# Optimization experiments

Measured on AMD Instinct MI355X. Metric: run time of the kernel, lower is better.

Reference implementation:

```python
import jax, jax.numpy as jnp
import numpy as np

N, F, H, E = 100000, 64, 8, 1200000
D = F // H
HID = 32  # hardcoded MLP hidden width in the module


def setup_inputs() -> dict:
    key = jax.random.key(0)
    ks = jax.random.split(key, 16)
    s = 0.05
    return {
        "h": jax.random.normal(ks[0], (N, F), jnp.float32),
        "W_src": jax.random.normal(ks[1], (F, F), jnp.float32) * s,
        "b_src": jnp.zeros((F,), jnp.float32),
        "W_dst": jax.random.normal(ks[2], (F, F), jnp.float32) * s,
        "b_dst": jnp.zeros((F,), jnp.float32),
        "Wa1_src": jax.random.normal(ks[3], (F, HID), jnp.float32) * s,
        "ba1_src": jnp.zeros((HID,), jnp.float32),
        "Wa2_src": jax.random.normal(ks[4], (HID, H), jnp.float32) * s,
        "ba2_src": jnp.zeros((H,), jnp.float32),
        "Wa1_dst": jax.random.normal(ks[5], (F, HID), jnp.float32) * s,
        "ba1_dst": jnp.zeros((HID,), jnp.float32),
        "Wa2_dst": jax.random.normal(ks[6], (HID, H), jnp.float32) * s,
        "ba2_dst": jnp.zeros((H,), jnp.float32),
        "edge_index": jax.random.randint(ks[7], (2, E), 0, N, jnp.int64),
    }


def _attn_mlp(x, W1, b1, W2, b2):
    # Sequential(LeakyReLU(0.2), Linear(F,32), LeakyReLU(0.2), Linear(32,H))
    y = jax.nn.leaky_relu(x, 0.2)
    y = y @ W1 + b1
    y = jax.nn.leaky_relu(y, 0.2)
    return y @ W2 + b2


def reference(h, W_src, b_src, W_dst, b_dst,
              Wa1_src, ba1_src, Wa2_src, ba2_src,
              Wa1_dst, ba1_dst, Wa2_dst, ba2_dst,
              edge_index):
    src, dst = edge_index[0], edge_index[1]
    g_src = h @ W_src + b_src          # [N,F]
    g_dst = h @ W_dst + b_dst          # [N,F]
    msg_src = g_src[src]               # [E,F] gather
    msg = msg_src + g_dst[dst]         # [E,F]
    a_src = jax.nn.sigmoid(_attn_mlp(msg, Wa1_src, ba1_src, Wa2_src, ba2_src))[:, :, None]    # [E,H,1]
    a_dst = jax.nn.sigmoid(_attn_mlp(g_dst, Wa1_dst, ba1_dst, Wa2_dst, ba2_dst))[:, :, None]  # [N,H,1]
    agg = jax.ops.segment_sum(a_src * msg_src.reshape(E, H, D), dst, num_segments=N)          # [N,H,D]
    h_next = a_dst * g_dst.reshape(N, H, D) + agg
    return h_next.reshape(N, F)
```

## Files before the change

kernel.cpp:

```cpp
#include <hip/hip_runtime.h>
#include <hip/hip_bf16.h>
#include <hip/hip_fp16.h>

#define NF   64
#define NH   8
#define ND   8
#define NHID 32
#define XS   68
#define OS   10

typedef __attribute__((ext_vector_type(8))) short bf16x8v;
typedef __attribute__((ext_vector_type(4))) float f32x4v;

__device__ __forceinline__ float bf2f(unsigned short u) {
    union { unsigned int i; float f; } v; v.i = ((unsigned int)u) << 16; return v.f;
}
__device__ __forceinline__ unsigned short f2bf(float f) {
    __hip_bfloat16 b = __float2bfloat16(f);
    union { __hip_bfloat16 b; unsigned short u; } v; v.b = b; return v.u;
}
__device__ __forceinline__ void unpack8(uint4 u, float* o) {
    o[0] = __uint_as_float(u.x << 16); o[1] = __uint_as_float(u.x & 0xffff0000u);
    o[2] = __uint_as_float(u.y << 16); o[3] = __uint_as_float(u.y & 0xffff0000u);
    o[4] = __uint_as_float(u.z << 16); o[5] = __uint_as_float(u.z & 0xffff0000u);
    o[6] = __uint_as_float(u.w << 16); o[7] = __uint_as_float(u.w & 0xffff0000u);
}
__device__ __forceinline__ uint4 pack8(const float* f) {
    uint4 u;
    u.x = (unsigned)f2bf(f[0]) | ((unsigned)f2bf(f[1]) << 16);
    u.y = (unsigned)f2bf(f[2]) | ((unsigned)f2bf(f[3]) << 16);
    u.z = (unsigned)f2bf(f[4]) | ((unsigned)f2bf(f[5]) << 16);
    u.w = (unsigned)f2bf(f[6]) | ((unsigned)f2bf(f[7]) << 16);
    return u;
}
__device__ __forceinline__ float leaky(float x) { return fmaxf(x, 0.2f * x); }
__device__ __forceinline__ float sigmoidf(float x) { return 1.f / (1.f + __expf(-x)); }

__global__ void detect_kernel(const int* __restrict__ edge, int* __restrict__ flags) {
    if (threadIdx.x == 0 && blockIdx.x == 0) {
        int oddnz = 0;
        for (int i = 0; i < 32; i++) oddnz |= edge[2 * i + 1];
        flags[0] = (oddnz == 0) ? 1 : 0;
    }
}

__device__ __forceinline__ void load_edge(const int* __restrict__ edge, int e, int E,
                                          int wide, int& s, int& d) {
    if (wide) { s = edge[2 * e]; d = edge[2 * (E + e)]; }
    else      { s = edge[e];     d = edge[E + e]; }
}

#define WBF_TOTAL 12544
__global__ __launch_bounds__(256) void prep_weights_kernel(
    const float* __restrict__ Ws, const float* __restrict__ Wd,
    const float* __restrict__ W1d, const float* __restrict__ W1s,
    const float* __restrict__ W2s, unsigned short* __restrict__ o)
{
    int i = blockIdx.x * 256 + threadIdx.x;
    float v;
    if (i < 4096)        { int j = i;         v = Ws [(j & 63) * 64 + (j >> 6)]; }
    else if (i < 8192)   { int j = i - 4096;  v = Wd [(j & 63) * 64 + (j >> 6)]; }
    else if (i < 10240)  { int j = i - 8192;  v = W1d[(j & 63) * 32 + (j >> 6)]; }
    else if (i < 12288)  { int j = i - 10240; v = W1s[(j & 63) * 32 + (j >> 6)]; }
    else if (i < 12544)  { int j = i - 12288; v = W2s[(j & 31) * 8  + (j >> 5)]; }
    else return;
    o[i] = f2bf(v);
}

__global__ __launch_bounds__(64) void node_mfma_kernel(
    const float* __restrict__ h,
    const unsigned short* __restrict__ WsT, const float* __restrict__ b_src,
    const unsigned short* __restrict__ WdT, const float* __restrict__ b_dst,
    const unsigned short* __restrict__ W1T, const float* __restrict__ ba1,
    const float* __restrict__ Wa2, const float* __restrict__ ba2,
    unsigned short* __restrict__ g_src_out, unsigned short* __restrict__ g_dst_out,
    float* __restrict__ out, int* __restrict__ counts, int N)
{
    __shared__ __align__(16) unsigned short sX[64 * XS];
    __shared__ __align__(16) unsigned short sY[64 * XS];
    __shared__ float sW2[NHID * NH];
    __shared__ float sb2[NH];

    int lane = threadIdx.x;
    int nsub = lane & 15, quad = lane >> 4;
    int base = blockIdx.x * 64;
    int n = base + lane;
    bool valid = n < N;
    size_t nn = valid ? (size_t)n : (size_t)(N - 1);

    if (valid && counts) counts[n] = 0;
    for (int i = lane; i < NHID * NH; i += 64) sW2[i] = Wa2[i];
    if (lane < NH) sb2[lane] = ba2[lane];

    {
        const float4* hv = (const float4*)(h + nn * NF);
        unsigned short* xrow = sX + lane * XS;
        #pragma unroll
        for (int k = 0; k < 8; k++) {
            float4 u0 = hv[2 * k], u1 = hv[2 * k + 1];
            float f[8] = { u0.x, u0.y, u0.z, u0.w, u1.x, u1.y, u1.z, u1.w };
            uint4 p = pack8(f);
            uint2* q = (uint2*)(xrow + k * 8);
            q[0] = make_uint2(p.x, p.y);
            q[1] = make_uint2(p.z, p.w);
        }
    }
    __syncthreads();

    #pragma unroll 1
    for (int m = 0; m < 2; m++) {
        const unsigned short* WT = m ? WdT : WsT;
        const float* bb = m ? b_dst : b_src;
        unsigned short* gout = m ? g_dst_out : g_src_out;

        bf16x8v Bf[2][4];
        #pragma unroll
        for (int ks = 0; ks < 2; ks++)
            #pragma unroll
            for (int nt = 0; nt < 4; nt++) {
                union { uint4 u; bf16x8v v; } u;
                u.u = *(const uint4*)(WT + (nt * 16 + nsub) * 64 + ks * 32 + quad * 8);
                Bf[ks][nt] = u.v;
            }

        f32x4v acc[4][4];
        #pragma unroll
        for (int mt = 0; mt < 4; mt++)
            #pragma unroll
            for (int nt = 0; nt < 4; nt++) {
                f32x4v z = {0.f, 0.f, 0.f, 0.f};
                acc[mt][nt] = z;
            }

        #pragma unroll
        for (int ks = 0; ks < 2; ks++)
            #pragma unroll
            for (int mt = 0; mt < 4; mt++) {
                const unsigned short* ap = sX + (mt * 16 + nsub) * XS + ks * 32 + quad * 8;
                union { uint2 d[2]; bf16x8v v; } ua;
                ua.d[0] = *(const uint2*)ap;
                ua.d[1] = *(const uint2*)(ap + 4);
                #pragma unroll
                for (int nt = 0; nt < 4; nt++)
                    acc[mt][nt] = __builtin_amdgcn_mfma_f32_16x16x32_bf16(
                        ua.v, Bf[ks][nt], acc[mt][nt], 0, 0, 0);
            }

        if (m == 1) __syncthreads();

        #pragma unroll
        for (int nt = 0; nt < 4; nt++) {
            float bv = bb[nt * 16 + nsub];
            #pragma unroll
            for (int mt = 0; mt < 4; mt++)
                #pragma unroll
                for (int r = 0; r < 4; r++)
                    sY[(mt * 16 + quad * 4 + r) * XS + nt * 16 + nsub] =
                        f2bf(acc[mt][nt][r] + bv);
        }
        __syncthreads();

        if (valid) {
            const unsigned short* yrow = sY + lane * XS;
            uint4* gp = (uint4*)(gout + (size_t)n * NF);
            #pragma unroll
            for (int k = 0; k < 8; k++) {
                uint2 a = *(const uint2*)(yrow + k * 8);
                uint2 b = *(const uint2*)(yrow + k * 8 + 4);
                gp[k] = make_uint4(a.x, a.y, b.x, b.y);
            }
        }
    }

    bf16x8v B1f[2][2];
    #pragma unroll
    for (int ks = 0; ks < 2; ks++)
        #pragma unroll
        for (int nt = 0; nt < 2; nt++) {
            union { uint4 u; bf16x8v v; } u;
            u.u = *(const uint4*)(W1T + (nt * 16 + nsub) * 64 + ks * 32 + quad * 8);
            B1f[ks][nt] = u.v;
        }

    f32x4v acc2[4][2];
    #pragma unroll
    for (int mt = 0; mt < 4; mt++)
        #pragma unroll
        for (int nt = 0; nt < 2; nt++) {
            f32x4v z = {0.f, 0.f, 0.f, 0.f};
            acc2[mt][nt] = z;
        }

    #pragma unroll
    for (int ks = 0; ks < 2; ks++)
        #pragma unroll
        for (int mt = 0; mt < 4; mt++) {
            const unsigned short* ap = sY + (mt * 16 + nsub) * XS + ks * 32 + quad * 8;
            uint2 d0 = *(const uint2*)ap;
            uint2 d1 = *(const uint2*)(ap + 4);
            float f[8];
            unpack8(make_uint4(d0.x, d0.y, d1.x, d1.y), f);
            #pragma unroll
            for (int t = 0; t < 8; t++) f[t] = leaky(f[t]);
            uint4 p = pack8(f);
            union { uint4 u; bf16x8v v; } ua; ua.u = p;
            #pragma unroll
            for (int nt = 0; nt < 2; nt++)
                acc2[mt][nt] = __builtin_amdgcn_mfma_f32_16x16x32_bf16(
                    ua.v, B1f[ks][nt], acc2[mt][nt], 0, 0, 0);
        }
    __syncthreads();

    #pragma unroll
    for (int nt = 0; nt < 2; nt++) {
        float b1v = ba1[nt * 16 + nsub];
        #pragma unroll
        for (int mt = 0; mt < 4; mt++)
            #pragma unroll
            for (int r = 0; r < 4; r++)
                sX[(mt * 16 + quad * 4 + r) * XS + nt * 16 + nsub] =
                    f2bf(leaky(acc2[mt][nt][r] + b1v));
    }
    __syncthreads();

    if (valid) {
        float hid[NHID];
        const unsigned short* hrow = sX + lane * XS;
        #pragma unroll
        for (int k = 0; k < 8; k++) {
            uint2 dv = *(const uint2*)(hrow + k * 4);
            hid[k * 4 + 0] = bf2f((unsigned short)(dv.x & 0xffffu));
            hid[k * 4 + 1] = bf2f((unsigned short)(dv.x >> 16));
            hid[k * 4 + 2] = bf2f((unsigned short)(dv.y & 0xffffu));
            hid[k * 4 + 3] = bf2f((unsigned short)(dv.y >> 16));
        }
        float a[NH];
        #pragma unroll
        for (int j = 0; j < NH; j++) a[j] = sb2[j];
        #pragma unroll
        for (int k = 0; k < NHID; k++) {
            float xk = hid[k];
            #pragma unroll
            for (int j = 0; j < NH; j++) a[j] = fmaf(xk, sW2[k * NH + j], a[j]);
        }
        #pragma unroll
        for (int j = 0; j < NH; j++) a[j] = sigmoidf(a[j]);

        const unsigned short* yrow = sY + lane * XS;
        float4* op = (float4*)(out + (size_t)n * NF);
        #pragma unroll
        for (int k = 0; k < 8; k++) {
            uint2 u0 = *(const uint2*)(yrow + k * 8);
            uint2 u1 = *(const uint2*)(yrow + k * 8 + 4);
            float g[8];
            unpack8(make_uint4(u0.x, u0.y, u1.x, u1.y), g);
            float ah0 = a[(k * 8) >> 3];
            op[2 * k]     = make_float4(ah0 * g[0], ah0 * g[1], ah0 * g[2], ah0 * g[3]);
            op[2 * k + 1] = make_float4(ah0 * g[4], ah0 * g[5], ah0 * g[6], ah0 * g[7]);
        }
    }
}

template <bool STORE_G>
__global__ __launch_bounds__(256) void node_kernel_t(
    const float* __restrict__ h,
    const float* __restrict__ W_src, const float* __restrict__ b_src,
    const float* __restrict__ W_dst, const float* __restrict__ b_dst,
    const float* __restrict__ Wa1, const float* __restrict__ ba1,
    const float* __restrict__ Wa2, const float* __restrict__ ba2,
    unsigned short* __restrict__ g_src_out, unsigned short* __restrict__ g_dst_out,
    float* __restrict__ out, int N)
{
    __shared__ __align__(16) float sWs[NF * NF];
    __shared__ __align__(16) float sWd[NF * NF];
    __shared__ __align__(16) float sW1[NF * NHID];
    __shared__ __align__(16) float sW2[NHID * NH];
    __shared__ float sbs[NF], sbd[NF], sb1[NHID], sb2[NH];

    int tid = threadIdx.x;
    for (int i = tid; i < NF * NF; i += 256) { sWs[i] = W_src[i]; sWd[i] = W_dst[i]; }
    for (int i = tid; i < NF * NHID; i += 256) sW1[i] = Wa1[i];
    if (tid < NHID * NH) sW2[tid] = Wa2[tid];
    if (tid < NF) { sbs[tid] = b_src[tid]; sbd[tid] = b_dst[tid]; }
    if (tid < NHID) sb1[tid] = ba1[tid];
    if (tid < NH) sb2[tid] = ba2[tid];
    __syncthreads();

    int n = blockIdx.x * 256 + tid;
    if (n >= N) return;

    float hrow[NF];
    const float4* hv = (const float4*)(h + (size_t)n * NF);
    #pragma unroll
    for (int k = 0; k < 16; k++) {
        float4 u = hv[k];
        hrow[k * 4 + 0] = u.x; hrow[k * 4 + 1] = u.y;
        hrow[k * 4 + 2] = u.z; hrow[k * 4 + 3] = u.w;
    }

    float acc[NF];
    const float4* Wsv = (const float4*)sWs;
    const float4* Wdv = (const float4*)sWd;

    if (STORE_G) {
        #pragma unroll
        for (int j = 0; j < NF; j++) acc[j] = sbs[j];
        for (int i = 0; i < NF; i++) {
            float hi = hrow[i];
            #pragma unroll
            for (int jb = 0; jb < 16; jb++) {
                float4 w = Wsv[i * 16 + jb];
                acc[jb * 4 + 0] = fmaf(hi, w.x, acc[jb * 4 + 0]);
                acc[jb * 4 + 1] = fmaf(hi, w.y, acc[jb * 4 + 1]);
                acc[jb * 4 + 2] = fmaf(hi, w.z, acc[jb * 4 + 2]);
                acc[jb * 4 + 3] = fmaf(hi, w.w, acc[jb * 4 + 3]);
            }
        }
        uint4* gs = (uint4*)(g_src_out + (size_t)n * NF);
        #pragma unroll
        for (int k = 0; k < 8; k++) gs[k] = pack8(acc + k * 8);
    }

    #pragma unroll
    for (int j = 0; j < NF; j++) acc[j] = sbd[j];
    for (int i = 0; i < NF; i++) {
        float hi = hrow[i];
        #pragma unroll
        for (int jb = 0; jb < 16; jb++) {
            float4 w = Wdv[i * 16 + jb];
            acc[jb * 4 + 0] = fmaf(hi, w.x, acc[jb * 4 + 0]);
            acc[jb * 4 + 1] = fmaf(hi, w.y, acc[jb * 4 + 1]);
            acc[jb * 4 + 2] = fmaf(hi, w.z, acc[jb * 4 + 2]);
            acc[jb * 4 + 3] = fmaf(hi, w.w, acc[jb * 4 + 3]);
        }
    }
    if (STORE_G) {
        uint4* gd = (uint4*)(g_dst_out + (size_t)n * NF);
        #pragma unroll
        for (int k = 0; k < 8; k++) gd[k] = pack8(acc + k * 8);
    }

    float hid[NHID];
    #pragma unroll
    for (int j = 0; j < NHID; j++) hid[j] = sb1[j];
    const float4* W1v = (const float4*)sW1;
    for (int i = 0; i < NF; i++) {
        float xi = leaky(acc[i]);
        #pragma unroll
        for (int jb = 0; jb < 8; jb++) {
            float4 w = W1v[i * 8 + jb];
            hid[jb * 4 + 0] = fmaf(xi, w.x, hid[jb * 4 + 0]);
            hid[jb * 4 + 1] = fmaf(xi, w.y, hid[jb * 4 + 1]);
            hid[jb * 4 + 2] = fmaf(xi, w.z, hid[jb * 4 + 2]);
            hid[jb * 4 + 3] = fmaf(xi, w.w, hid[jb * 4 + 3]);
        }
    }
    float a[NH];
    #pragma unroll
    for (int j = 0; j < NH; j++) a[j] = sb2[j];
    #pragma unroll
    for (int k = 0; k < NHID; k++) {
        float xk = leaky(hid[k]);
        #pragma unroll
        for (int j = 0; j < NH; j++) a[j] = fmaf(xk, sW2[k * NH + j], a[j]);
    }
    #pragma unroll
    for (int j = 0; j < NH; j++) a[j] = sigmoidf(a[j]);

    float4* ap = (float4*)(out + (size_t)n * NF);
    #pragma unroll
    for (int k = 0; k < 16; k++) {
        int j = k * 4;
        ap[k] = make_float4(a[(j + 0) >> 3] * acc[j + 0],
                            a[(j + 1) >> 3] * acc[j + 1],
                            a[(j + 2) >> 3] * acc[j + 2],
                            a[(j + 3) >> 3] * acc[j + 3]);
    }
}

__global__ __launch_bounds__(256) void hist_kernel(
    const int* __restrict__ edge, const int* __restrict__ flags,
    int* __restrict__ counts, int* __restrict__ rank, int E, int N)
{
    int e = blockIdx.x * 256 + threadIdx.x;
    if (e >= E) return;
    int s, d;
    load_edge(edge, e, E, flags[0], s, d);
    if ((unsigned)s >= (unsigned)N || (unsigned)d >= (unsigned)N) { rank[e] = -1; return; }
    rank[e] = atomicAdd(&counts[d], 1);
}

__global__ __launch_bounds__(256) void scan1_kernel(
    const int* __restrict__ counts, int* __restrict__ offsets,
    int* __restrict__ bsums, int N)
{
    __shared__ int lds[256];
    int tid = threadIdx.x;
    int base = blockIdx.x * 2048 + tid * 8;
    int v[8]; int s = 0;
    #pragma unroll
    for (int k = 0; k < 8; k++) { int idx = base + k; int t = (idx < N) ? counts[idx] : 0; v[k] = t; s += t; }
    lds[tid] = s;
    __syncthreads();
    for (int off = 1; off < 256; off <<= 1) {
        int y = (tid >= off) ? lds[tid - off] : 0;
        __syncthreads();
        lds[tid] += y;
        __syncthreads();
    }
    int run = lds[tid] - s;
    #pragma unroll
    for (int k = 0; k < 8; k++) { int idx = base + k; if (idx < N) offsets[idx] = run; run += v[k]; }
    if (tid == 255) bsums[blockIdx.x] = lds[255];
}

__global__ void scan2_kernel(int* __restrict__ bsums, int* __restrict__ offsets, int NB, int N) {
    if (threadIdx.x == 0 && blockIdx.x == 0) {
        int run = 0;
        for (int i = 0; i < NB; i++) { int t = bsums[i]; bsums[i] = run; run += t; }
        offsets[N] = run;
    }
}

__global__ __launch_bounds__(256) void scan3_kernel(
    int* __restrict__ offsets, const int* __restrict__ bsums, int N)
{
    int add = bsums[blockIdx.x];
    int base = blockIdx.x * 2048 + threadIdx.x * 8;
    #pragma unroll
    for (int k = 0; k < 8; k++) { int idx = base + k; if (idx < N) offsets[idx] += add; }
}

__global__ __launch_bounds__(256) void scatter_kernel(
    const int* __restrict__ edge, const int* __restrict__ flags,
    const int* __restrict__ offsets, const int* __restrict__ rank,
    uint2* __restrict__ sorted_sd, int E, int N)
{
    int e = blockIdx.x * 256 + threadIdx.x;
    if (e >= E) return;
    int r = rank[e];
    if (r < 0) return;
    int s, d;
    load_edge(edge, e, E, flags[0], s, d);
    int pos = offsets[d] + r;
    sorted_sd[pos] = make_uint2((unsigned)s, (unsigned)d);
}

__global__ __launch_bounds__(256) void edge_mlp_mfma_kernel(
    const uint2* __restrict__ sorted_sd, const int* __restrict__ total_p,
    const unsigned short* __restrict__ g_src, const unsigned short* __restrict__ g_dst,
    const unsigned short* __restrict__ W1T, const float* __restrict__ ba1,
    const unsigned short* __restrict__ W2T, const float* __restrict__ ba2,
    __half* __restrict__ a_sorted)
{
    __shared__ __align__(16) unsigned short sX[4 * 64 * XS];
    __shared__ __align__(16) __half sOut[4 * 64 * OS];
    __shared__ float sb1[NHID], sb2[NH];

    int tid = threadIdx.x;
    if (tid < NHID) sb1[tid] = ba1[tid];
    if (tid < NH) sb2[tid] = ba2[tid];

    int wave = tid >> 6;
    int lane = tid & 63;
    int nsub = lane & 15;
    int quad = lane >> 4;
    int total = *total_p;
    int i = blockIdx.x * 256 + wave * 64 + lane;
    bool valid = i < total;
    uint2 sd = valid ? sorted_sd[i] : make_uint2(0u, 0u);

    unsigned short* xrow = sX + (wave * 64 + lane) * XS;
    {
        const uint4* gs = (const uint4*)(g_src + (size_t)sd.x * NF);
        const uint4* gd = (const uint4*)(g_dst + (size_t)sd.y * NF);
        #pragma unroll
        for (int k = 0; k < 8; k++) {
            float A8[8], B8[8], x8[8];
            unpack8(gs[k], A8); unpack8(gd[k], B8);
            #pragma unroll
            for (int t = 0; t < 8; t++) x8[t] = leaky(A8[t] + B8[t]);
            uint4 pk = pack8(x8);
            uint2* q = (uint2*)(xrow + k * 8);
            q[0] = make_uint2(pk.x, pk.y);
            q[1] = make_uint2(pk.z, pk.w);
        }
    }

    bf16x8v Bf[2][2];
    #pragma unroll
    for (int ks = 0; ks < 2; ks++)
        #pragma unroll
        for (int nt = 0; nt < 2; nt++) {
            union { uint4 u; bf16x8v v; } u;
            u.u = *(const uint4*)(W1T + (nt * 16 + nsub) * 64 + ks * 32 + quad * 8);
            Bf[ks][nt] = u.v;
        }
    bf16x8v B2f;
    {
        union { uint4 u; bf16x8v v; } u;
        if (nsub < NH) u.u = *(const uint4*)(W2T + nsub * 32 + quad * 8);
        else           u.u = make_uint4(0u, 0u, 0u, 0u);
        B2f = u.v;
    }

    __syncthreads();

    f32x4v acc[4][2];
    #pragma unroll
    for (int mt = 0; mt < 4; mt++)
        #pragma unroll
        for (int nt = 0; nt < 2; nt++) {
            f32x4v z = {0.f, 0.f, 0.f, 0.f};
            acc[mt][nt] = z;
        }

    const unsigned short* wbase = sX + wave * 64 * XS;
    #pragma unroll
    for (int ks = 0; ks < 2; ks++) {
        #pragma unroll
        for (int mt = 0; mt < 4; mt++) {
            const unsigned short* ap = wbase + (mt * 16 + nsub) * XS + ks * 32 + quad * 8;
            union { uint2 d[2]; bf16x8v v; } ua;
            ua.d[0] = *(const uint2*)ap;
            ua.d[1] = *(const uint2*)(ap + 4);
            #pragma unroll
            for (int nt = 0; nt < 2; nt++)
                acc[mt][nt] = __builtin_amdgcn_mfma_f32_16x16x32_bf16(
                    ua.v, Bf[ks][nt], acc[mt][nt], 0, 0, 0);
        }
    }

    __syncthreads();

    #pragma unroll
    for (int nt = 0; nt < 2; nt++) {
        int n = nt * 16 + nsub;
        float b1v = sb1[n];
        #pragma unroll
        for (int mt = 0; mt < 4; mt++) {
            #pragma unroll
            for (int r = 0; r < 4; r++) {
                int m = mt * 16 + quad * 4 + r;
                sX[(wave * 64 + m) * XS + n] = f2bf(leaky(acc[mt][nt][r] + b1v));
            }
        }
    }

    __syncthreads();

    f32x4v acc2[4];
    #pragma unroll
    for (int mt = 0; mt < 4; mt++) { f32x4v z = {0.f, 0.f, 0.f, 0.f}; acc2[mt] = z; }
    #pragma unroll
    for (int mt = 0; mt < 4; mt++) {
        const unsigned short* ap = wbase + (mt * 16 + nsub) * XS + quad * 8;
        union { uint2 d[2]; bf16x8v v; } ua;
        ua.d[0] = *(const uint2*)ap;
        ua.d[1] = *(const uint2*)(ap + 4);
        acc2[mt] = __builtin_amdgcn_mfma_f32_16x16x32_bf16(ua.v, B2f, acc2[mt], 0, 0, 0);
    }

    if (nsub < NH) {
        float b2v = sb2[nsub];
        #pragma unroll
        for (int mt = 0; mt < 4; mt++)
            #pragma unroll
            for (int r = 0; r < 4; r++) {
                int m = mt * 16 + quad * 4 + r;
                sOut[(wave * 64 + m) * OS + nsub] = __float2half(sigmoidf(acc2[mt][r] + b2v));
            }
    }
    __syncthreads();

    if (valid) {
        const unsigned int* orow = (const unsigned int*)(sOut + (wave * 64 + lane) * OS);
        uint4 pk = make_uint4(orow[0], orow[1], orow[2], orow[3]);
        *(uint4*)(a_sorted + (size_t)i * NH) = pk;
    }
}

__global__ __launch_bounds__(256) void aggregate_kernel(
    const int* __restrict__ offsets, const uint2* __restrict__ sorted_sd,
    const __half* __restrict__ a_sorted, const unsigned short* __restrict__ g_src,
    float* __restrict__ out, int N)
{
    int d = blockIdx.x * 32 + (threadIdx.x >> 3);
    if (d >= N) return;
    int l = threadIdx.x & 7;
    int beg = offsets[d], end = offsets[d + 1];

    float acc[8] = {0.f, 0.f, 0.f, 0.f, 0.f, 0.f, 0.f, 0.f};
    int i = beg;
    for (; i + 2 <= end; i += 2) {
        unsigned s0 = sorted_sd[i].x;
        unsigned s1 = sorted_sd[i + 1].x;
        float av0 = __half2float(a_sorted[(size_t)i * NH + l]);
        float av1 = __half2float(a_sorted[(size_t)(i + 1) * NH + l]);
        uint4 q0 = *(const uint4*)(g_src + (size_t)s0 * NF + l * 8);
        uint4 q1 = *(const uint4*)(g_src + (size_t)s1 * NF + l * 8);
        float f0[8], f1[8];
        unpack8(q0, f0); unpack8(q1, f1);
        #pragma unroll
        for (int t = 0; t < 8; t++) acc[t] = fmaf(av0, f0[t], acc[t]);
        #pragma unroll
        for (int t = 0; t < 8; t++) acc[t] = fmaf(av1, f1[t], acc[t]);
    }
    if (i < end) {
        unsigned s0 = sorted_sd[i].x;
        float av0 = __half2float(a_sorted[(size_t)i * NH + l]);
        uint4 q0 = *(const uint4*)(g_src + (size_t)s0 * NF + l * 8);
        float f0[8]; unpack8(q0, f0);
        #pragma unroll
        for (int t = 0; t < 8; t++) acc[t] = fmaf(av0, f0[t], acc[t]);
    }

    float4* o4 = (float4*)(out + (size_t)d * NF + l * 8);
    float4 v0 = o4[0], v1 = o4[1];
    v0.x += acc[0]; v0.y += acc[1]; v0.z += acc[2]; v0.w += acc[3];
    v1.x += acc[4]; v1.y += acc[5]; v1.z += acc[6]; v1.w += acc[7];
    o4[0] = v0; o4[1] = v1;
}

__global__ __launch_bounds__(256) void edge_kernel(
    const int* __restrict__ edge, const int* __restrict__ flags,
    const unsigned short* __restrict__ g_src, const unsigned short* __restrict__ g_dst,
    const float* __restrict__ Wa1, const float* __restrict__ ba1,
    const float* __restrict__ Wa2, const float* __restrict__ ba2,
    float* __restrict__ out, int E, int N)
{
    __shared__ __align__(16) float sW1[NF * NHID];
    __shared__ __align__(16) float sW2[NHID * NH];
    __shared__ float sb1[NHID], sb2[NH];
    int tid = threadIdx.x;
    for (int i = tid; i < NF * NHID; i += 256) sW1[i] = Wa1[i];
    if (tid < NHID * NH) sW2[tid] = Wa2[tid];
    if (tid < NHID) sb1[tid] = ba1[tid];
    if (tid < NH) sb2[tid] = ba2[tid];
    __syncthreads();

    int e = blockIdx.x * 256 + tid;
    if (e >= E) return;
    int s, d;
    load_edge(edge, e, E, flags[0], s, d);
    if ((unsigned)s >= (unsigned)N || (unsigned)d >= (unsigned)N) return;

    float ms[NF];
    float hid[NHID];
    #pragma unroll
    for (int j = 0; j < NHID; j++) hid[j] = sb1[j];

    const uint4* gs = (const uint4*)(g_src + (size_t)s * NF);
    const uint4* gd = (const uint4*)(g_dst + (size_t)d * NF);
    #pragma unroll
    for (int k = 0; k < 8; k++) {
        float a8[8], b8[8];
        unpack8(gs[k], a8);
        unpack8(gd[k], b8);
        #pragma unroll
        for (int t = 0; t < 8; t++) {
            int i = k * 8 + t;
            ms[i] = a8[t];
            float x = leaky(a8[t] + b8[t]);
            #pragma unroll
            for (int j = 0; j < NHID; j++) hid[j] = fmaf(x, sW1[i * NHID + j], hid[j]);
        }
    }

    float a[NH];
    #pragma unroll
    for (int j = 0; j < NH; j++) a[j] = sb2[j];
    #pragma unroll
    for (int k = 0; k < NHID; k++) {
        float xk = leaky(hid[k]);
        #pragma unroll
        for (int j = 0; j < NH; j++) a[j] = fmaf(xk, sW2[k * NH + j], a[j]);
    }

    float* arow = out + (size_t)d * NF;
    #pragma unroll
    for (int hh = 0; hh < NH; hh++) {
        float ah = sigmoidf(a[hh]);
        #pragma unroll
        for (int dd = 0; dd < ND; dd++)
            unsafeAtomicAdd(arow + hh * ND + dd, ah * ms[hh * ND + dd]);
    }
}

__global__ __launch_bounds__(256) void edge_kernel_fused(
    const int* __restrict__ edge, const int* __restrict__ flags,
    const float* __restrict__ h,
    const float* __restrict__ W_src, const float* __restrict__ b_src,
    const float* __restrict__ W_dst, const float* __restrict__ b_dst,
    const float* __restrict__ Wa1, const float* __restrict__ ba1,
    const float* __restrict__ Wa2, const float* __restrict__ ba2,
    float* __restrict__ out, int E, int N)
{
    __shared__ __align__(16) float sWs[NF * NF];
    __shared__ __align__(16) float sWd[NF * NF];
    __shared__ __align__(16) float sW1[NF * NHID];
    __shared__ __align__(16) float sW2[NHID * NH];
    __shared__ float sbs[NF], sbd[NF], sb1[NHID], sb2[NH];
    int tid = threadIdx.x;
    for (int i = tid; i < NF * NF; i += 256) { sWs[i] = W_src[i]; sWd[i] = W_dst[i]; }
    for (int i = tid; i < NF * NHID; i += 256) sW1[i] = Wa1[i];
    if (tid < NHID * NH) sW2[tid] = Wa2[tid];
    if (tid < NF) { sbs[tid] = b_src[tid]; sbd[tid] = b_dst[tid]; }
    if (tid < NHID) sb1[tid] = ba1[tid];
    if (tid < NH) sb2[tid] = ba2[tid];
    __syncthreads();

    int e = blockIdx.x * 256 + tid;
    if (e >= E) return;
    int wide = flags ? flags[0] : 0;
    int s, d;
    load_edge(edge, e, E, wide, s, d);
    if ((unsigned)s >= (unsigned)N || (unsigned)d >= (unsigned)N) return;

    float gsr[NF], msg[NF];
    {
        float hrow[NF];
        #pragma unroll
        for (int i = 0; i < NF; i++) hrow[i] = h[(size_t)s * NF + i];
        #pragma unroll
        for (int j = 0; j < NF; j++) gsr[j] = sbs[j];
        for (int i = 0; i < NF; i++) {
            float hi = hrow[i];
            #pragma unroll
            for (int j = 0; j < NF; j++) gsr[j] = fmaf(hi, sWs[i * NF + j], gsr[j]);
        }
    }
    #pragma unroll
    for (int j = 0; j < NF; j++) msg[j] = gsr[j] + sbd[j];
    for (int i = 0; i < NF; i++) {
        float hi = h[(size_t)d * NF + i];
        #pragma unroll
        for (int j = 0; j < NF; j++) msg[j] = fmaf(hi, sWd[i * NF + j], msg[j]);
    }

    float hid[NHID];
    #pragma unroll
    for (int j = 0; j < NHID; j++) hid[j] = sb1[j];
    for (int i = 0; i < NF; i++) {
        float x = leaky(msg[i]);
        #pragma unroll
        for (int j = 0; j < NHID; j++) hid[j] = fmaf(x, sW1[i * NHID + j], hid[j]);
    }
    float a[NH];
    #pragma unroll
    for (int j = 0; j < NH; j++) a[j] = sb2[j];
    #pragma unroll
    for (int k = 0; k < NHID; k++) {
        float xk = leaky(hid[k]);
        #pragma unroll
        for (int j = 0; j < NH; j++) a[j] = fmaf(xk, sW2[k * NH + j], a[j]);
    }

    float* arow = out + (size_t)d * NF;
    #pragma unroll
    for (int hh = 0; hh < NH; hh++) {
        float ah = sigmoidf(a[hh]);
        #pragma unroll
        for (int dd = 0; dd < ND; dd++)
            unsafeAtomicAdd(arow + hh * ND + dd, ah * gsr[hh * ND + dd]);
    }
}

static inline size_t al256(size_t x) { return (x + 255) & ~(size_t)255; }

extern "C" void kernel_launch(void* const* d_in, const int* in_sizes, int n_in,
                              void* d_out, int out_size, void* d_ws, size_t ws_size,
                              hipStream_t stream) {
    const float* h       = (const float*)d_in[0];
    const float* W_src   = (const float*)d_in[1];
    const float* b_src   = (const float*)d_in[2];
    const float* W_dst   = (const float*)d_in[3];
    const float* b_dst   = (const float*)d_in[4];
    const float* Wa1_src = (const float*)d_in[5];
    const float* ba1_src = (const float*)d_in[6];
    const float* Wa2_src = (const float*)d_in[7];
    const float* ba2_src = (const float*)d_in[8];
    const float* Wa1_dst = (const float*)d_in[9];
    const float* ba1_dst = (const float*)d_in[10];
    const float* Wa2_dst = (const float*)d_in[11];
    const float* ba2_dst = (const float*)d_in[12];
    const int* edge = (const int*)d_in[13];

    int N = in_sizes[0] / NF;
    int E = in_sizes[13] / 2;
    float* out = (float*)d_out;

    int nodeBlocks = (N + 255) / 256;
    int nodeWaves  = (N + 63) / 64;
    int edgeBlocks = (E + 255) / 256;
    int NB1 = (N + 2047) / 2048;

    size_t o_flags  = 0;
    size_t o_wbf    = al256(o_flags + 256);
    size_t o_gsrc   = al256(o_wbf + (size_t)WBF_TOTAL * 2);
    size_t o_gdst   = al256(o_gsrc + (size_t)N * NF * 2);
    size_t o_asort  = al256(o_gdst + (size_t)N * NF * 2);
    size_t o_counts = al256(o_asort + (size_t)E * NH * 2);
    size_t o_offs   = al256(o_counts + (size_t)N * 4);
    size_t o_bsums  = al256(o_offs + ((size_t)N + 1) * 4);
    size_t o_sorted = al256(o_bsums + (size_t)NB1 * 4);
    size_t need     = o_sorted + (size_t)E * 8;

    size_t gB = (size_t)N * NF * 2;

    if (ws_size >= need) {
        char* w = (char*)d_ws;
        int*            flags   = (int*)(w + o_flags);
        unsigned short* wbf     = (unsigned short*)(w + o_wbf);
        unsigned short* WsT     = wbf;
        unsigned short* WdT     = wbf + 4096;
        unsigned short* W1dT    = wbf + 8192;
        unsigned short* W1sT    = wbf + 10240;
        unsigned short* W2sT    = wbf + 12288;
        unsigned short* g_src   = (unsigned short*)(w + o_gsrc);
        unsigned short* g_dst   = (unsigned short*)(w + o_gdst);
        __half*         a_sort  = (__half*)(w + o_asort);
        int*            rank    = (int*)(w + o_asort);
        int*            counts  = (int*)(w + o_counts);
        int*            offsets = (int*)(w + o_offs);
        int*            bsums   = (int*)(w + o_bsums);
        uint2*          sorted  = (uint2*)(w + o_sorted);

        detect_kernel<<<1, 1, 0, stream>>>(edge, flags);
        prep_weights_kernel<<<(WBF_TOTAL + 255) / 256, 256, 0, stream>>>(
            W_src, W_dst, Wa1_dst, Wa1_src, Wa2_src, wbf);

        node_mfma_kernel<<<nodeWaves, 64, 0, stream>>>(
            h, WsT, b_src, WdT, b_dst,
            W1dT, ba1_dst, Wa2_dst, ba2_dst,
            g_src, g_dst, out, counts, N);

        hist_kernel<<<edgeBlocks, 256, 0, stream>>>(edge, flags, counts, rank, E, N);

        scan1_kernel<<<NB1, 256, 0, stream>>>(counts, offsets, bsums, N);
        scan2_kernel<<<1, 1, 0, stream>>>(bsums, offsets, NB1, N);
        scan3_kernel<<<NB1, 256, 0, stream>>>(offsets, bsums, N);

        scatter_kernel<<<edgeBlocks, 256, 0, stream>>>(
            edge, flags, offsets, rank, sorted, E, N);

        edge_mlp_mfma_kernel<<<edgeBlocks, 256, 0, stream>>>(
            sorted, offsets + N, g_src, g_dst,
            W1sT, ba1_src, W2sT, ba2_src, a_sort);

        aggregate_kernel<<<(N + 31) / 32, 256, 0, stream>>>(
            offsets, sorted, a_sort, g_src, out, N);
    } else if (ws_size >= 256 + 2 * gB) {
        int* flags = (int*)d_ws;
        unsigned short* g_src = (unsigned short*)((char*)d_ws + 256);
        unsigned short* g_dst = g_src + (size_t)N * NF;

        detect_kernel<<<1, 1, 0, stream>>>(edge, flags);

        node_kernel_t<true><<<nodeBlocks, 256, 0, stream>>>(
            h, W_src, b_src, W_dst, b_dst,
            Wa1_dst, ba1_dst, Wa2_dst, ba2_dst,
            g_src, g_dst, out, N);

        edge_kernel<<<edgeBlocks, 256, 0, stream>>>(
            edge, flags, g_src, g_dst,
            Wa1_src, ba1_src, Wa2_src, ba2_src,
            out, E, N);
    } else {
        int* flags = (ws_size >= 256) ? (int*)d_ws : nullptr;
        if (flags) detect_kernel<<<1, 1, 0, stream>>>(edge, flags);

        node_kernel_t<false><<<nodeBlocks, 256, 0, stream>>>(
            h, W_src, b_src, W_dst, b_dst,
            Wa1_dst, ba1_dst, Wa2_dst, ba2_dst,
            nullptr, nullptr, out, N);

        edge_kernel_fused<<<edgeBlocks, 256, 0, stream>>>(
            edge, flags, h,
            W_src, b_src, W_dst, b_dst,
            Wa1_src, ba1_src, Wa2_src, ba2_src,
            out, E, N);
    }
}
```

Before: 288.5 us.

## Fuse edge histogram into node kernel and split sorted edge arrays

Moves the per-destination edge histogram into the tail of the node MFMA kernel, and moves zeroing of counts into the weight-prep kernel. This removes one kernel launch and lets the atomics overlap with node work. The sorted (src,dst) pair array becomes separate src and dst int arrays: scatter writes only src, a new fill kernel writes dst per segment, and aggregate reads only 4 bytes per edge. In exchange there is an extra launch, the fill kernel is serialized per node, and the fused histogram loop runs on small 64-thread blocks.

```diff
diff --git a/kernel.cpp b/kernel.cpp
--- a/kernel.cpp
+++ b/kernel.cpp
@@ -54,9 +54,11 @@
 __global__ __launch_bounds__(256) void prep_weights_kernel(
     const float* __restrict__ Ws, const float* __restrict__ Wd,
     const float* __restrict__ W1d, const float* __restrict__ W1s,
-    const float* __restrict__ W2s, unsigned short* __restrict__ o)
+    const float* __restrict__ W2s, unsigned short* __restrict__ o,
+    int* __restrict__ counts, int N)
 {
     int i = blockIdx.x * 256 + threadIdx.x;
+    if (i < N) counts[i] = 0;
     float v;
     if (i < 4096)        { int j = i;         v = Ws [(j & 63) * 64 + (j >> 6)]; }
     else if (i < 8192)   { int j = i - 4096;  v = Wd [(j & 63) * 64 + (j >> 6)]; }
@@ -74,7 +76,9 @@
     const unsigned short* __restrict__ W1T, const float* __restrict__ ba1,
     const float* __restrict__ Wa2, const float* __restrict__ ba2,
     unsigned short* __restrict__ g_src_out, unsigned short* __restrict__ g_dst_out,
-    float* __restrict__ out, int* __restrict__ counts, int N)
+    float* __restrict__ out,
+    const int* __restrict__ edge, const int* __restrict__ flags,
+    int* __restrict__ counts, int* __restrict__ rank, int E, int N)
 {
     __shared__ __align__(16) unsigned short sX[64 * XS];
     __shared__ __align__(16) unsigned short sY[64 * XS];
@@ -88,7 +92,6 @@
     bool valid = n < N;
     size_t nn = valid ? (size_t)n : (size_t)(N - 1);
 
-    if (valid && counts) counts[n] = 0;
     for (int i = lane; i < NHID * NH; i += 64) sW2[i] = Wa2[i];
     if (lane < NH) sb2[lane] = ba2[lane];
 
@@ -259,6 +262,17 @@
             op[2 * k + 1] = make_float4(ah0 * g[4], ah0 * g[5], ah0 * g[6], ah0 * g[7]);
         }
     }
+
+    {
+        int wide = flags[0];
+        int stride = gridDim.x * 64;
+        for (int e = blockIdx.x * 64 + lane; e < E; e += stride) {
+            int s, d;
+            load_edge(edge, e, E, wide, s, d);
+            if ((unsigned)s >= (unsigned)N || (unsigned)d >= (unsigned)N) { rank[e] = -1; continue; }
+            rank[e] = atomicAdd(&counts[d], 1);
+        }
+    }
 }
 
 template <bool STORE_G>
@@ -378,18 +392,6 @@
     }
 }
 
-__global__ __launch_bounds__(256) void hist_kernel(
-    const int* __restrict__ edge, const int* __restrict__ flags,
-    int* __restrict__ counts, int* __restrict__ rank, int E, int N)
-{
-    int e = blockIdx.x * 256 + threadIdx.x;
-    if (e >= E) return;
-    int s, d;
-    load_edge(edge, e, E, flags[0], s, d);
-    if ((unsigned)s >= (unsigned)N || (unsigned)d >= (unsigned)N) { rank[e] = -1; return; }
-    rank[e] = atomicAdd(&counts[d], 1);
-}
-
 __global__ __launch_bounds__(256) void scan1_kernel(
     const int* __restrict__ counts, int* __restrict__ offsets,
     int* __restrict__ bsums, int N)
@@ -434,7 +436,7 @@
 __global__ __launch_bounds__(256) void scatter_kernel(
     const int* __restrict__ edge, const int* __restrict__ flags,
     const int* __restrict__ offsets, const int* __restrict__ rank,
-    uint2* __restrict__ sorted_sd, int E, int N)
+    int* __restrict__ sorted_s, int E, int N)
 {
     int e = blockIdx.x * 256 + threadIdx.x;
     if (e >= E) return;
@@ -442,12 +444,21 @@
     if (r < 0) return;
     int s, d;
     load_edge(edge, e, E, flags[0], s, d);
-    int pos = offsets[d] + r;
-    sorted_sd[pos] = make_uint2((unsigned)s, (unsigned)d);
+    sorted_s[offsets[d] + r] = s;
+}
+
+__global__ __launch_bounds__(256) void fill_d_kernel(
+    const int* __restrict__ offsets, int* __restrict__ sorted_d, int N)
+{
+    int d = blockIdx.x * 256 + threadIdx.x;
+    if (d >= N) return;
+    int beg = offsets[d], end = offsets[d + 1];
+    for (int i = beg; i < end; i++) sorted_d[i] = d;
 }
 
 __global__ __launch_bounds__(256) void edge_mlp_mfma_kernel(
-    const uint2* __restrict__ sorted_sd, const int* __restrict__ total_p,
+    const int* __restrict__ sorted_s, const int* __restrict__ sorted_d,
+    const int* __restrict__ total_p,
     const unsigned short* __restrict__ g_src, const unsigned short* __restrict__ g_dst,
     const unsigned short* __restrict__ W1T, const float* __restrict__ ba1,
     const unsigned short* __restrict__ W2T, const float* __restrict__ ba2,
@@ -468,12 +479,13 @@
     int total = *total_p;
     int i = blockIdx.x * 256 + wave * 64 + lane;
     bool valid = i < total;
-    uint2 sd = valid ? sorted_sd[i] : make_uint2(0u, 0u);
+    int s = valid ? sorted_s[i] : 0;
+    int d = valid ? sorted_d[i] : 0;
 
     unsigned short* xrow = sX + (wave * 64 + lane) * XS;
     {
-        const uint4* gs = (const uint4*)(g_src + (size_t)sd.x * NF);
-        const uint4* gd = (const uint4*)(g_dst + (size_t)sd.y * NF);
+        const uint4* gs = (const uint4*)(g_src + (size_t)s * NF);
+        const uint4* gd = (const uint4*)(g_dst + (size_t)d * NF);
         #pragma unroll
         for (int k = 0; k < 8; k++) {
             float A8[8], B8[8], x8[8];
@@ -581,7 +593,7 @@
 }
 
 __global__ __launch_bounds__(256) void aggregate_kernel(
-    const int* __restrict__ offsets, const uint2* __restrict__ sorted_sd,
+    const int* __restrict__ offsets, const int* __restrict__ sorted_s,
     const __half* __restrict__ a_sorted, const unsigned short* __restrict__ g_src,
     float* __restrict__ out, int N)
 {
@@ -593,8 +605,8 @@
     float acc[8] = {0.f, 0.f, 0.f, 0.f, 0.f, 0.f, 0.f, 0.f};
     int i = beg;
     for (; i + 2 <= end; i += 2) {
-        unsigned s0 = sorted_sd[i].x;
-        unsigned s1 = sorted_sd[i + 1].x;
+        int s0 = sorted_s[i];
+        int s1 = sorted_s[i + 1];
         float av0 = __half2float(a_sorted[(size_t)i * NH + l]);
         float av1 = __half2float(a_sorted[(size_t)(i + 1) * NH + l]);
         uint4 q0 = *(const uint4*)(g_src + (size_t)s0 * NF + l * 8);
@@ -607,7 +619,7 @@
         for (int t = 0; t < 8; t++) acc[t] = fmaf(av1, f1[t], acc[t]);
     }
     if (i < end) {
-        unsigned s0 = sorted_sd[i].x;
+        int s0 = sorted_s[i];
         float av0 = __half2float(a_sorted[(size_t)i * NH + l]);
         uint4 q0 = *(const uint4*)(g_src + (size_t)s0 * NF + l * 8);
         float f0[8]; unpack8(q0, f0);
@@ -794,6 +806,7 @@
     int nodeWaves  = (N + 63) / 64;
     int edgeBlocks = (E + 255) / 256;
     int NB1 = (N + 2047) / 2048;
+    int prepN = (N > WBF_TOTAL ? N : WBF_TOTAL);
 
     size_t o_flags  = 0;
     size_t o_wbf    = al256(o_flags + 256);
@@ -824,32 +837,34 @@
         int*            counts  = (int*)(w + o_counts);
         int*            offsets = (int*)(w + o_offs);
         int*            bsums   = (int*)(w + o_bsums);
-        uint2*          sorted  = (uint2*)(w + o_sorted);
+        int*            sorted_s = (int*)(w + o_sorted);
+        int*            sorted_d = sorted_s + E;
 
         detect_kernel<<<1, 1, 0, stream>>>(edge, flags);
-        prep_weights_kernel<<<(WBF_TOTAL + 255) / 256, 256, 0, stream>>>(
-            W_src, W_dst, Wa1_dst, Wa1_src, Wa2_src, wbf);
+        prep_weights_kernel<<<(prepN + 255) / 256, 256, 0, stream>>>(
+            W_src, W_dst, Wa1_dst, Wa1_src, Wa2_src, wbf, counts, N);
 
         node_mfma_kernel<<<nodeWaves, 64, 0, stream>>>(
             h, WsT, b_src, WdT, b_dst,
             W1dT, ba1_dst, Wa2_dst, ba2_dst,
-            g_src, g_dst, out, counts, N);
-
-        hist_kernel<<<edgeBlocks, 256, 0, stream>>>(edge, flags, counts, rank, E, N);
+            g_src, g_dst, out,
+            edge, flags, counts, rank, E, N);
 
         scan1_kernel<<<NB1, 256, 0, stream>>>(counts, offsets, bsums, N);
         scan2_kernel<<<1, 1, 0, stream>>>(bsums, offsets, NB1, N);
         scan3_kernel<<<NB1, 256, 0, stream>>>(offsets, bsums, N);
 
         scatter_kernel<<<edgeBlocks, 256, 0, stream>>>(
-            edge, flags, offsets, rank, sorted, E, N);
+            edge, flags, offsets, rank, sorted_s, E, N);
+
+        fill_d_kernel<<<nodeBlocks, 256, 0, stream>>>(offsets, sorted_d, N);
 
         edge_mlp_mfma_kernel<<<edgeBlocks, 256, 0, stream>>>(
-            sorted, offsets + N, g_src, g_dst,
+            sorted_s, sorted_d, offsets + N, g_src, g_dst,
             W1sT, ba1_src, W2sT, ba2_src, a_sort);
 
         aggregate_kernel<<<(N + 31) / 32, 256, 0, stream>>>(
-            offsets, sorted, a_sort, g_src, out, N);
+            offsets, sorted_s, a_sort, g_src, out, N);
     } else if (ws_size >= 256 + 2 * gB) {
         int* flags = (int*)d_ws;
         unsigned short* g_src = (unsigned short*)((char*)d_ws + 256);
```

Measured after the change: 297.1 us. +3.0%, slower.
